# Kernel tuning notes

Hardware: AMD Instinct MI355X
Metric: run time of the kernel (lower is better)

The kernel has to match this reference:

```python
import jax, jax.numpy as jnp
import numpy as np

TOPK = 10
NUM_CLASSES = 80
ALPHA = 1.0
BETA = 6.0
EPS = 1e-9
IOU_EPS = 1e-7
IMG = 640.0


def setup_inputs() -> dict:
    key = jax.random.key(0)
    ks = jax.random.split(key, 8)
    B, N, M, C = 8, 16800, 96, NUM_CLASSES
    pd_scores = jax.random.normal(ks[0], (B, N, C), dtype=jnp.float32)
    # predicted boxes: valid xyxy around random centers
    p_c = jax.random.uniform(ks[1], (B, N, 2), dtype=jnp.float32) * IMG
    p_wh = jax.random.uniform(ks[2], (B, N, 2), dtype=jnp.float32) * (IMG / 8.0) + 1.0
    pd_bboxes = jnp.concatenate([p_c - p_wh / 2, p_c + p_wh / 2], axis=-1)
    anchor_points = jax.random.uniform(ks[3], (N, 2), dtype=jnp.float32) * IMG
    gt_labels = jax.random.randint(ks[4], (B, M, 1), 0, C, dtype=jnp.int32)
    g_c = jax.random.uniform(ks[5], (B, M, 2), dtype=jnp.float32) * IMG
    g_wh = jax.random.uniform(ks[6], (B, M, 2), dtype=jnp.float32) * (IMG / 4.0) + 4.0
    gt_bboxes = jnp.concatenate([g_c - g_wh / 2, g_c + g_wh / 2], axis=-1)
    # first 72 of 96 GT slots valid per image (padding mask)
    mask_gt = jnp.broadcast_to((jnp.arange(M) < 72).astype(jnp.float32)[None, :, None], (B, M, 1))
    return {"pd_scores": pd_scores, "pd_bboxes": pd_bboxes, "anchor_points": anchor_points,
            "gt_labels": gt_labels, "gt_bboxes": gt_bboxes, "mask_gt": mask_gt}


def _bbox_iou(b1, b2):
    # b1: (B,N,1,4), b2: (B,1,M,4) -> (B,N,M)
    ix1 = jnp.maximum(b1[..., 0], b2[..., 0])
    iy1 = jnp.maximum(b1[..., 1], b2[..., 1])
    ix2 = jnp.minimum(b1[..., 2], b2[..., 2])
    iy2 = jnp.minimum(b1[..., 3], b2[..., 3])
    inter = jnp.clip(ix2 - ix1, 0.0) * jnp.clip(iy2 - iy1, 0.0)
    a1 = (b1[..., 2] - b1[..., 0]) * (b1[..., 3] - b1[..., 1])
    a2 = (b2[..., 2] - b2[..., 0]) * (b2[..., 3] - b2[..., 1])
    return inter / (a1 + a2 - inter + IOU_EPS)


def _assign(pd_scores, pd_bboxes, anchor_points, gt_labels, gt_bboxes, mask_gt):
    B, N, C = pd_scores.shape
    M = gt_bboxes.shape[1]
    mg = mask_gt[:, :, 0]                      # (B,M)
    gl = gt_labels[:, :, 0].astype(jnp.int32)  # (B,M)

    # --- anchor centers inside GT boxes -> (B,N,M) ---
    lt = gt_bboxes[:, :, None, :2]             # (B,M,1,2)
    rb = gt_bboxes[:, :, None, 2:]
    ap = anchor_points[None, None, :, :]       # (1,1,N,2)
    deltas = jnp.concatenate([ap - lt, rb - ap], axis=-1)  # (B,M,N,4)
    mask_in_gts = jnp.swapaxes(deltas.min(-1) > EPS, 1, 2).astype(pd_scores.dtype)  # (B,N,M)

    # --- IoU + alignment metric ---
    overlaps = jnp.clip(_bbox_iou(pd_bboxes[:, :, None, :], gt_bboxes[:, None, :, :]), 0.0)  # (B,N,M)
    gl_exp = jnp.broadcast_to(gl[:, None, :], (B, N, M))
    bbox_scores = jnp.take_along_axis(pd_scores, gl_exp, axis=2)  # (B,N,M)
    align = (jax.nn.sigmoid(bbox_scores) ** ALPHA) * (overlaps ** BETA)
    align = align * mg[:, None, :]

    # --- top-k anchors per GT (over anchor axis) ---
    mT = jnp.swapaxes(align, 1, 2)                     # (B,M,N)
    topk_vals, topk_idxs = jax.lax.top_k(mT, min(TOPK, N))
    keep = topk_vals.max(-1, keepdims=True) > EPS       # (B,M,1)
    bi = jnp.arange(B)[:, None, None]
    mi = jnp.arange(M)[None, :, None]
    sel = jnp.zeros((B, M, N), dtype=bool).at[bi, mi, topk_idxs].set(True)
    mask_topk = jnp.swapaxes(sel & keep, 1, 2).astype(pd_scores.dtype)  # (B,N,M)

    mask_pos = mask_in_gts * mask_topk * mg[:, None, :]

    # --- resolve anchors assigned to multiple GTs by max IoU ---
    fg_count = mask_pos.sum(2)                          # (B,N)
    multi = (fg_count[:, :, None] > 1)
    is_max = jax.nn.one_hot(overlaps.argmax(2), M, dtype=overlaps.dtype)
    mask_pos = jnp.where(multi, is_max, mask_pos)
    fg_mask = mask_pos.sum(2) > 0                       # (B,N) bool
    target_gt_idx = mask_pos.argmax(2)                  # (B,N)

    # --- gather targets ---
    target_labels = jnp.take_along_axis(gl, target_gt_idx, axis=1)
    target_labels = jnp.clip(target_labels, 0, C - 1)
    target_bboxes = jnp.take_along_axis(gt_bboxes, target_gt_idx[:, :, None], axis=1)  # (B,N,4)

    # --- normalized alignment metric -> scores (faithful .long() truncation) ---
    max_per_gt = jnp.clip(align.max(1, keepdims=True), EPS)
    norm_align = (align / max_per_gt).max(2) * fg_mask.astype(align.dtype)  # (B,N)
    bi2 = jnp.arange(B)[:, None]
    ni = jnp.arange(N)[None, :]
    assigned = jnp.zeros((B, N, C), dtype=jnp.int32).at[bi2, ni, target_labels].set(
        norm_align.astype(jnp.int32))
    target_scores = jnp.where(fg_mask[:, :, None], assigned.astype(pd_scores.dtype),
                              jnp.zeros((), pd_scores.dtype))
    return target_bboxes, target_scores, fg_mask, target_gt_idx


def reference(pd_scores, pd_bboxes, anchor_points, gt_labels, gt_bboxes, mask_gt):
    return _assign(pd_scores, pd_bboxes, anchor_points, gt_labels, gt_bboxes, mask_gt)
```

## Files before the change

### kernel.cpp

```cpp
#include <hip/hip_runtime.h>
#include <math.h>

#define TOPK_K 10
#define EPS_F 1e-9f
#define IOU_EPS_F 1e-7f
#define CH 128
#define QH 4
#define CCH 256
#define MGMAX 32

struct Iou6 { float ov; float ov6; };

__device__ __forceinline__ Iou6 iou_pow6(float px1, float py1, float px2, float py2,
                                         float gx1, float gy1, float gx2, float gy2) {
#pragma clang fp contract(off)
  float ix1 = fmaxf(px1, gx1);
  float iy1 = fmaxf(py1, gy1);
  float ix2 = fminf(px2, gx2);
  float iy2 = fminf(py2, gy2);
  float dw = fmaxf(ix2 - ix1, 0.0f);
  float dh = fmaxf(iy2 - iy1, 0.0f);
  float inter = dw * dh;
  float a1 = (px2 - px1) * (py2 - py1);
  float a2 = (gx2 - gx1) * (gy2 - gy1);
  float den = a1 + a2 - inter + IOU_EPS_F;
  float iou = inter / den;
  float ov = fmaxf(iou, 0.0f);
  float ov2 = ov * ov;
  Iou6 r; r.ov = ov; r.ov6 = ov2 * ov2 * ov2;
  return r;
}

__device__ __forceinline__ float sigmoid_f(float x) {
#pragma clang fp contract(off)
  return 1.0f / (1.0f + expf(-x));
}

__device__ __forceinline__ unsigned long long mk_key(float v, int idx) {
  if (idx < 0) return 0ull;
  unsigned uv = __float_as_uint(v) | 0x80000000u;
  return ((unsigned long long)uv << 32) | (unsigned)(~idx);
}

#define KINSERT(kk)                                                      \
  if ((kk) > kl[9]) {                                                    \
    _Pragma("unroll")                                                    \
    for (int j = 9; j >= 1; --j) {                                       \
      if ((kk) > kl[j - 1])      kl[j] = kl[j - 1];                      \
      else if ((kk) > kl[j])     kl[j] = (kk);                           \
    }                                                                    \
    if ((kk) > kl[0]) kl[0] = (kk);                                      \
  }

#define WAVE_MERGE10()                                                         \
  {                                                                            \
    _Pragma("unroll")                                                          \
    for (int r = 0; r < TOPK_K; ++r) {                                         \
      unsigned long long kmine = kl[0], kw = kl[0];                            \
      _Pragma("unroll")                                                        \
      for (int off = 32; off > 0; off >>= 1) {                                 \
        unsigned long long o = __shfl_xor(kw, off);                            \
        if (o > kw) kw = o;                                                    \
      }                                                                        \
      if (lane == 0) skey[wid * TOPK_K + r] = kw;                              \
      if (kmine == kw && kw != 0ull) {                  \
        _Pragma("unroll")                                                      \
        for (int j = 0; j < TOPK_K - 1; ++j) kl[j] = kl[j + 1];                \
        kl[TOPK_K - 1] = 0ull;                                                 \
      }                                                                        \
    }                                                                          \
  }

#define FINAL_MERGE10()                                                        \
  {                                                                            \
    _Pragma("unroll")                                                          \
    for (int r = 0; r < TOPK_K; ++r) {                                         \
      unsigned long long kmine = kl[0], kw = kl[0];                            \
      _Pragma("unroll")                                                        \
      for (int off = 32; off > 0; off >>= 1) {                                 \
        unsigned long long o = __shfl_xor(kw, off);                            \
        if (o > kw) kw = o;                                                    \
      }                                                                        \
      if (r == 0) maxv = __uint_as_float((unsigned)(kw >> 32) & 0x7fffffffu);  \
      if (r == TOPK_K - 1) {                                                   \
        Tv = __uint_as_float((unsigned)(kw >> 32) & 0x7fffffffu);              \
        Ti = (int)~(unsigned)(kw & 0xffffffffu);                               \
      }                                                                        \
      if (kmine == kw && kw != 0ull) {                                         \
        _Pragma("unroll")                                                      \
        for (int j = 0; j < TOPK_K - 1; ++j) kl[j] = kl[j + 1];                \
        kl[TOPK_K - 1] = 0ull;                                                 \
      }                                                                        \
    }                                                                          \
  }

__launch_bounds__(CCH)
__global__ void k_collect(const float* __restrict__ pd_scores,
                          const float* __restrict__ pd_bboxes,
                          const int*   __restrict__ gt_labels,
                          const float* __restrict__ gt_bboxes,
                          const float* __restrict__ mask_gt,
                          int B, int N, int M, int C, int CAP, int MGS,
                          int*    __restrict__ cnt,
                          float2* __restrict__ lists)
{
  const int b = blockIdx.z;
  const int m0 = blockIdx.y * MGS;
  const int mcount = min(MGS, M - m0);
  const int tid = threadIdx.x;
  const int n = blockIdx.x * CCH + tid;
  const int lane = tid & 63;
  const int wid  = tid >> 6;
  const bool valid = (n < N);

  __shared__ float4             sgt[MGMAX];
  __shared__ int                sgl[MGMAX];
  __shared__ int                smg[MGMAX];
  __shared__ unsigned long long sbal[CCH / 64][MGMAX];
  __shared__ int                wbase[CCH / 64][MGMAX];

  if (tid < mcount) {
    sgt[tid] = *(const float4*)(gt_bboxes + (size_t)(b * M + m0 + tid) * 4);
    sgl[tid] = min(max(gt_labels[b * M + m0 + tid], 0), C - 1);
    smg[tid] = (mask_gt[b * M + m0 + tid] > 0.0f) ? 1 : 0;
  }
  __syncthreads();

  float4 p = make_float4(-1.f, -1.f, -2.f, -2.f);
  if (valid) p = *(const float4*)(pd_bboxes + ((size_t)b * N + n) * 4);

  for (int mi = 0; mi < mcount; ++mi) {
    const float4 g = sgt[mi];
    bool pred = false;
    if (smg[mi]) {
      float ix1 = fmaxf(p.x, g.x), iy1 = fmaxf(p.y, g.y);
      float ix2 = fminf(p.z, g.z), iy2 = fminf(p.w, g.w);
      pred = (ix2 > ix1) && (iy2 > iy1);
    }
    unsigned long long bal = __ballot(pred);
    if (lane == 0) sbal[wid][mi] = bal;
  }
  __syncthreads();

  if (tid < mcount) {
    int t0 = __popcll(sbal[0][tid]), t1 = __popcll(sbal[1][tid]);
    int t2 = __popcll(sbal[2][tid]), t3 = __popcll(sbal[3][tid]);
    int tot = t0 + t1 + t2 + t3;
    int gb = (tot > 0) ? atomicAdd(&cnt[b * M + m0 + tid], tot) : 0;
    wbase[0][tid] = gb;
    wbase[1][tid] = gb + t0;
    wbase[2][tid] = gb + t0 + t1;
    wbase[3][tid] = gb + t0 + t1 + t2;
  }
  __syncthreads();

  const float* __restrict__ srow = pd_scores + ((size_t)b * N + n) * C;
  const unsigned long long ltm = (1ull << lane) - 1ull;
  for (int mi = 0; mi < mcount; ++mi) {
    unsigned long long bal = sbal[wid][mi];
    if (bal == 0ull) continue;
    if ((bal >> lane) & 1ull) {
      int pos = wbase[wid][mi] + __popcll(bal & ltm);
      if (pos < CAP) {
        const float4 g = sgt[mi];
        Iou6 io = iou_pow6(p.x, p.y, p.z, p.w, g.x, g.y, g.z, g.w);
        float a = sigmoid_f(srow[sgl[mi]]) * io.ov6;
        lists[(size_t)(b * M + m0 + mi) * CAP + pos] = make_float2(a, __int_as_float(n));
      }
    }
  }
}

__launch_bounds__(256)
__global__ void k_select(const float* __restrict__ pd_scores,
                         const float* __restrict__ pd_bboxes,
                         const int*   __restrict__ gt_labels,
                         const float* __restrict__ gt_bboxes,
                         const float* __restrict__ mask_gt,
                         int B, int N, int M, int C, int CAP,
                         const int*    __restrict__ cnt,
                         const float2* __restrict__ lists,
                         float* __restrict__ maxv_out,
                         float* __restrict__ t10v_out,
                         int*   __restrict__ t10i_out)
{
  const int m = blockIdx.x, b = blockIdx.y;
  const int bm = b * M + m;
  const int tid = threadIdx.x;
  const int lane = tid & 63;
  const int wid  = tid >> 6;

  __shared__ unsigned long long skey[4 * TOPK_K];
  __shared__ int sfb;

  if (mask_gt[bm] == 0.0f) {
    if (tid == 0) { maxv_out[bm] = 0.0f; t10v_out[bm] = 0.0f; t10i_out[bm] = -1; }
    return;
  }

  unsigned long long kl[TOPK_K];
#pragma unroll
  for (int j = 0; j < TOPK_K; ++j) kl[j] = 0ull;

  float maxv = 0.0f, Tv = 0.0f; int Ti = -1;
  const int c = cnt[bm];
  bool fb = (c < TOPK_K) || (c > CAP);

  if (!fb) {
    const float2* __restrict__ lp = lists + (size_t)bm * CAP;
    for (int i = tid; i < c; i += 256) {
      float2 e = lp[i];
      unsigned long long k = mk_key(e.x, __float_as_int(e.y));
      KINSERT(k);
    }
    WAVE_MERGE10();
    __syncthreads();
    if (wid == 0) {
#pragma unroll
      for (int j = 0; j < TOPK_K; ++j) kl[j] = 0ull;
      kl[0] = (lane < 4 * TOPK_K) ? skey[lane] : 0ull;
      FINAL_MERGE10();
      if (lane == 0) sfb = (Tv == 0.0f) ? 1 : 0;
    }
    __syncthreads();
    fb = (sfb != 0);
  }

  if (fb) {
#pragma unroll
    for (int j = 0; j < TOPK_K; ++j) kl[j] = 0ull;
    const float4 g = *(const float4*)(gt_bboxes + (size_t)bm * 4);
    int gl = min(max(gt_labels[bm], 0), C - 1);
    const float* __restrict__ srow = pd_scores + (size_t)b * N * C;
    const float4* __restrict__ pb = (const float4*)(pd_bboxes + (size_t)b * N * 4);
    for (int n = tid; n < N; n += 256) {
      float4 p = pb[n];
      Iou6 io = iou_pow6(p.x, p.y, p.z, p.w, g.x, g.y, g.z, g.w);
      unsigned long long kub = mk_key(io.ov6, 0);
      if (kub > kl[TOPK_K - 1]) {
        float a = (io.ov6 == 0.0f) ? 0.0f
                                   : sigmoid_f(srow[(size_t)n * C + gl]) * io.ov6;
        unsigned long long k = mk_key(a, n);
        KINSERT(k);
      }
    }
    __syncthreads();
    WAVE_MERGE10();
    __syncthreads();
    if (wid == 0) {
#pragma unroll
      for (int j = 0; j < TOPK_K; ++j) kl[j] = 0ull;
      kl[0] = (lane < 4 * TOPK_K) ? skey[lane] : 0ull;
      FINAL_MERGE10();
    }
  }

  if (tid == 0) { maxv_out[bm] = maxv; t10v_out[bm] = Tv; t10i_out[bm] = Ti; }
}

__launch_bounds__(512)
__global__ void k_assign(const float* __restrict__ pd_scores,
                         const float* __restrict__ pd_bboxes,
                         const float* __restrict__ anchors,
                         const int*   __restrict__ gt_labels,
                         const float* __restrict__ gt_bboxes,
                         const float* __restrict__ mask_gt,
                         const float* __restrict__ maxv_in,
                         const float* __restrict__ t10v_in,
                         const int*   __restrict__ t10i_in,
                         int B, int N, int M, int C,
                         float* __restrict__ out)
{
  const int b = blockIdx.y;
  const int chunk0 = blockIdx.x * CH;
  const int tid = threadIdx.x;
  const int al = tid & (CH - 1);
  const int qr = tid >> 7;
  const int n = chunk0 + al;

  __shared__ float4 sgt[128];
  __shared__ int    sgl[128];
  __shared__ float  smg[128];
  __shared__ float  smpg[128];
  __shared__ float  spre[128];
  __shared__ float  smT[128];
  __shared__ int    smI[128];
  __shared__ int    skeep[128];
  __shared__ float  s_pov[QH - 1][CH];
  __shared__ int    s_parg[QH - 1][CH], s_pcnt[QH - 1][CH],
                    s_pfirst[QH - 1][CH], s_pone[QH - 1][CH];
  __shared__ int    slab[CH];
  __shared__ float  ssv[CH];

  if (tid < M) {
    sgt[tid] = *(const float4*)(gt_bboxes + (size_t)(b * M + tid) * 4);
    sgl[tid] = min(max(gt_labels[b * M + tid], 0), C - 1);
    smg[tid] = mask_gt[b * M + tid];
    float mv  = maxv_in[b * M + tid];
    float mpg = fmaxf(mv, EPS_F);
    smpg[tid] = mpg;
    spre[tid] = mpg * 0.999999f;
    smT[tid]  = t10v_in[b * M + tid];
    smI[tid]  = t10i_in[b * M + tid];
    skeep[tid] = (mv > EPS_F) ? 1 : 0;
  }
  __syncthreads();

  float* __restrict__ out_bbox   = out;
  float* __restrict__ out_scores = out + (size_t)B * N * 4;
  float* __restrict__ out_fg     = out_scores + (size_t)B * N * C;
  float* __restrict__ out_tgt    = out_fg + (size_t)B * N;

  const bool valid = (n < N);
  float pov = -1.0f; int parg = 0;
  int pcnt = 0, pfirst = -1, pone = 0;

  if (valid) {
    const float4 p = *(const float4*)(pd_bboxes + ((size_t)b * N + n) * 4);
    const float ax = anchors[(size_t)n * 2];
    const float ay = anchors[(size_t)n * 2 + 1];
    const float* __restrict__ srow = pd_scores + ((size_t)b * N + n) * C;

    const int mq  = (M + QH - 1) / QH;
    const int mlo = qr * mq;
    const int mhi = min(M, mlo + mq);

    for (int m = mlo; m < mhi; ++m) {
      const float4 gbb = sgt[m];
      Iou6 io = iou_pow6(p.x, p.y, p.z, p.w, gbb.x, gbb.y, gbb.z, gbb.w);
      if (io.ov > pov) { pov = io.ov; parg = m; }
      const float mgv = smg[m];
      if (mgv > 0.0f) {
        const float T = smT[m];
        const int keep = skeep[m];
        bool mem = false;
        const bool cand = keep && (io.ov6 > T);
        if (cand || (io.ov6 >= spre[m])) {
          const float a = sigmoid_f(srow[sgl[m]]) * io.ov6;
          if (cand) mem = (a > T) || (a == T && n <= smI[m]);
          if (a / smpg[m] >= 1.0f) pone = 1;
        } else if (keep && (T == 0.0f) && (io.ov6 == 0.0f)) {
          mem = (n <= smI[m]);
        }
        if (mem) {
          const float d = fminf(fminf(ax - gbb.x, ay - gbb.y),
                                fminf(gbb.z - ax, gbb.w - ay));
          if (d > EPS_F) { pcnt++; if (pfirst < 0) pfirst = m; }
        }
      }
    }
  }

  if (qr >= 1 && valid) {
    s_pov[qr - 1][al] = pov; s_parg[qr - 1][al] = parg; s_pcnt[qr - 1][al] = pcnt;
    s_pfirst[qr - 1][al] = pfirst; s_pone[qr - 1][al] = pone;
  }
  __syncthreads();

  if (qr == 0 && valid) {
#pragma unroll
    for (int q = 0; q < QH - 1; ++q) {
      float ovq = s_pov[q][al];
      if (ovq > pov) { pov = ovq; parg = s_parg[q][al]; }
      pcnt += s_pcnt[q][al];
      if (pfirst < 0) pfirst = s_pfirst[q][al];
      pone |= s_pone[q][al];
    }

    float fg; int tgt;
    if (pcnt > 1)       { fg = 1.0f; tgt = parg; }
    else if (pcnt == 1) { fg = 1.0f; tgt = pfirst; }
    else                { fg = 0.0f; tgt = 0; }

    slab[al] = sgl[tgt];
    ssv[al]  = (fg > 0.0f && pone) ? 1.0f : 0.0f;

    *(float4*)(out_bbox + ((size_t)b * N + n) * 4) = sgt[tgt];
    out_fg[(size_t)b * N + n]  = fg;
    out_tgt[(size_t)b * N + n] = (float)tgt;
  }
  __syncthreads();

  const int rows = min(CH, N - chunk0);
  const int c4n = C >> 2;
  float4* __restrict__ os4 = (float4*)(out_scores + ((size_t)b * N + chunk0) * C);
  const int tot = rows * c4n;
  if (c4n == 20) {
    for (int i = tid; i < tot; i += 512) {
      unsigned row = __umulhi((unsigned)i, 0xCCCCCCCDu) >> 4;
      int c0 = (i - (int)row * 20) * 4;
      int lr = slab[row]; float v = ssv[row];
      float4 o;
      o.x = (c0     == lr) ? v : 0.0f;
      o.y = (c0 + 1 == lr) ? v : 0.0f;
      o.z = (c0 + 2 == lr) ? v : 0.0f;
      o.w = (c0 + 3 == lr) ? v : 0.0f;
      os4[i] = o;
    }
  } else {
    for (int i = tid; i < tot; i += 512) {
      int row = i / c4n;
      int c0 = (i - row * c4n) * 4;
      int lr = slab[row]; float v = ssv[row];
      float4 o;
      o.x = (c0     == lr) ? v : 0.0f;
      o.y = (c0 + 1 == lr) ? v : 0.0f;
      o.z = (c0 + 2 == lr) ? v : 0.0f;
      o.w = (c0 + 3 == lr) ? v : 0.0f;
      os4[i] = o;
    }
  }
}

extern "C" void kernel_launch(void* const* d_in, const int* in_sizes, int n_in,
                              void* d_out, int out_size, void* d_ws, size_t ws_size,
                              hipStream_t stream) {
  const float* pd_scores = (const float*)d_in[0];
  const float* pd_bboxes = (const float*)d_in[1];
  const float* anchors   = (const float*)d_in[2];
  const int*   gt_labels = (const int*)d_in[3];
  const float* gt_bboxes = (const float*)d_in[4];
  const float* mask_gt   = (const float*)d_in[5];

  const int N = in_sizes[2] / 2;
  const int B = in_sizes[1] / (N * 4);
  const int M = in_sizes[3] / B;
  const int C = in_sizes[0] / (B * N);
  const int BM = B * M;

  char* ws = (char*)d_ws;
  float*  maxv  = (float*)ws;  ws += (size_t)BM * 4;
  float*  t10v  = (float*)ws;  ws += (size_t)BM * 4;
  int*    t10i  = (int*)ws;    ws += (size_t)BM * 4;
  int*    cnt   = (int*)ws;    ws += (size_t)BM * 4;
  float2* lists = (float2*)ws;

  const size_t header = (size_t)BM * 16;
  size_t avail = (ws_size > header) ? (ws_size - header) : 0;
  long long capll = (long long)(avail / ((size_t)BM * 8));
  int CAP = (int)((capll > 4096) ? 4096 : capll);
  if (CAP < 512) CAP = 0;

  hipMemsetAsync(cnt, 0, (size_t)BM * 4, stream);

  if (CAP > 0) {
    int MGRP = 4;
    int MGS  = (M + MGRP - 1) / MGRP;
    while (MGS > MGMAX) { MGRP *= 2; MGS = (M + MGRP - 1) / MGRP; }
    dim3 gc((N + CCH - 1) / CCH, MGRP, B);
    k_collect<<<gc, CCH, 0, stream>>>(pd_scores, pd_bboxes, gt_labels, gt_bboxes,
                                      mask_gt, B, N, M, C, CAP, MGS, cnt, lists);
  }

  dim3 gs(M, B);
  k_select<<<gs, 256, 0, stream>>>(pd_scores, pd_bboxes, gt_labels, gt_bboxes,
                                   mask_gt, B, N, M, C, CAP, cnt, lists,
                                   maxv, t10v, t10i);

  dim3 g2((N + CH - 1) / CH, B);
  k_assign<<<g2, 512, 0, stream>>>(pd_scores, pd_bboxes, anchors, gt_labels,
                                   gt_bboxes, mask_gt, maxv, t10v, t10i,
                                   B, N, M, C, (float*)d_out);
}
```

Before: 80.41 us.

## Replace atomic candidate lists with per-wave fixed slots in collect/select

The collect kernel no longer reserves space in each GT's candidate list with global atomicAdd, and the count-buffer memset is gone. Instead, each wavefront writes its candidates into a private 32-entry slot per GT and records its own count. This removes two block barriers, the atomics and one memset launch. The select kernel now walks the per-wave slots and counts, and falls back to a full scan when any slot overflows or there are too few candidates. The cost is a much larger workspace, a fallback if the workspace is too small, and uneven per-thread serial loops in select.

New measurement: 88.51 us. 10.1% more time.

```diff
diff --git a/kernel.cpp b/kernel.cpp
--- a/kernel.cpp
+++ b/kernel.cpp
@@ -8,6 +8,7 @@
 #define QH 4
 #define CCH 256
 #define MGMAX 32
+#define SLOT 32
 
 struct Iou6 { float ov; float ov6; };
 
@@ -100,8 +101,8 @@
                           const int*   __restrict__ gt_labels,
                           const float* __restrict__ gt_bboxes,
                           const float* __restrict__ mask_gt,
-                          int B, int N, int M, int C, int CAP, int MGS,
-                          int*    __restrict__ cnt,
+                          int B, int N, int M, int C, int MGS, int WPG,
+                          int*    __restrict__ wcount,
                           float2* __restrict__ lists)
 {
   const int b = blockIdx.z;
@@ -111,13 +112,11 @@
   const int n = blockIdx.x * CCH + tid;
   const int lane = tid & 63;
   const int wid  = tid >> 6;
-  const bool valid = (n < N);
-
-  __shared__ float4             sgt[MGMAX];
-  __shared__ int                sgl[MGMAX];
-  __shared__ int                smg[MGMAX];
-  __shared__ unsigned long long sbal[CCH / 64][MGMAX];
-  __shared__ int                wbase[CCH / 64][MGMAX];
+  const int slot = blockIdx.x * (CCH / 64) + wid;
+
+  __shared__ float4 sgt[MGMAX];
+  __shared__ int    sgl[MGMAX];
+  __shared__ int    smg[MGMAX];
 
   if (tid < mcount) {
     sgt[tid] = *(const float4*)(gt_bboxes + (size_t)(b * M + m0 + tid) * 4);
@@ -127,7 +126,10 @@
   __syncthreads();
 
   float4 p = make_float4(-1.f, -1.f, -2.f, -2.f);
-  if (valid) p = *(const float4*)(pd_bboxes + ((size_t)b * N + n) * 4);
+  if (n < N) p = *(const float4*)(pd_bboxes + ((size_t)b * N + n) * 4);
+
+  const float* __restrict__ srow = pd_scores + ((size_t)b * N + n) * C;
+  const unsigned long long ltm = (1ull << lane) - 1ull;
 
   for (int mi = 0; mi < mcount; ++mi) {
     const float4 g = sgt[mi];
@@ -138,34 +140,14 @@
       pred = (ix2 > ix1) && (iy2 > iy1);
     }
     unsigned long long bal = __ballot(pred);
-    if (lane == 0) sbal[wid][mi] = bal;
-  }
-  __syncthreads();
-
-  if (tid < mcount) {
-    int t0 = __popcll(sbal[0][tid]), t1 = __popcll(sbal[1][tid]);
-    int t2 = __popcll(sbal[2][tid]), t3 = __popcll(sbal[3][tid]);
-    int tot = t0 + t1 + t2 + t3;
-    int gb = (tot > 0) ? atomicAdd(&cnt[b * M + m0 + tid], tot) : 0;
-    wbase[0][tid] = gb;
-    wbase[1][tid] = gb + t0;
-    wbase[2][tid] = gb + t0 + t1;
-    wbase[3][tid] = gb + t0 + t1 + t2;
-  }
-  __syncthreads();
-
-  const float* __restrict__ srow = pd_scores + ((size_t)b * N + n) * C;
-  const unsigned long long ltm = (1ull << lane) - 1ull;
-  for (int mi = 0; mi < mcount; ++mi) {
-    unsigned long long bal = sbal[wid][mi];
-    if (bal == 0ull) continue;
-    if ((bal >> lane) & 1ull) {
-      int pos = wbase[wid][mi] + __popcll(bal & ltm);
-      if (pos < CAP) {
-        const float4 g = sgt[mi];
+    const size_t sbase = (size_t)(b * M + m0 + mi) * WPG + slot;
+    if (lane == 0 && slot < WPG) wcount[sbase] = __popcll(bal);
+    if (pred) {
+      int pos = __popcll(bal & ltm);
+      if (pos < SLOT) {
         Iou6 io = iou_pow6(p.x, p.y, p.z, p.w, g.x, g.y, g.z, g.w);
         float a = sigmoid_f(srow[sgl[mi]]) * io.ov6;
-        lists[(size_t)(b * M + m0 + mi) * CAP + pos] = make_float2(a, __int_as_float(n));
+        lists[sbase * SLOT + pos] = make_float2(a, __int_as_float(n));
       }
     }
   }
@@ -177,8 +159,8 @@
                          const int*   __restrict__ gt_labels,
                          const float* __restrict__ gt_bboxes,
                          const float* __restrict__ mask_gt,
-                         int B, int N, int M, int C, int CAP,
-                         const int*    __restrict__ cnt,
+                         int B, int N, int M, int C, int WPG,
+                         const int*    __restrict__ wcount,
                          const float2* __restrict__ lists,
                          float* __restrict__ maxv_out,
                          float* __restrict__ t10v_out,
@@ -191,7 +173,7 @@
   const int wid  = tid >> 6;
 
   __shared__ unsigned long long skey[4 * TOPK_K];
-  __shared__ int sfb;
+  __shared__ int sTot, sOvf, sfb;
 
   if (mask_gt[bm] == 0.0f) {
     if (tid == 0) { maxv_out[bm] = 0.0f; t10v_out[bm] = 0.0f; t10i_out[bm] = -1; }
@@ -203,27 +185,42 @@
   for (int j = 0; j < TOPK_K; ++j) kl[j] = 0ull;
 
   float maxv = 0.0f, Tv = 0.0f; int Ti = -1;
-  const int c = cnt[bm];
-  bool fb = (c < TOPK_K) || (c > CAP);
+  bool fb = (WPG <= 0);
 
   if (!fb) {
-    const float2* __restrict__ lp = lists + (size_t)bm * CAP;
-    for (int i = tid; i < c; i += 256) {
-      float2 e = lp[i];
-      unsigned long long k = mk_key(e.x, __float_as_int(e.y));
-      KINSERT(k);
-    }
-    WAVE_MERGE10();
+    if (tid == 0) { sTot = 0; sOvf = 0; }
     __syncthreads();
-    if (wid == 0) {
+    int mytot = 0, myovf = 0;
+    for (int s = tid; s < WPG; s += 256) {
+      int c = wcount[(size_t)bm * WPG + s];
+      mytot += c;
+      if (c > SLOT) myovf = 1;
+      const float2* __restrict__ lp = lists + ((size_t)bm * WPG + s) * SLOT;
+      int cc = min(c, SLOT);
+      for (int i = 0; i < cc; ++i) {
+        float2 e = lp[i];
+        unsigned long long k = mk_key(e.x, __float_as_int(e.y));
+        KINSERT(k);
+      }
+    }
+    if (mytot) atomicAdd(&sTot, mytot);
+    if (myovf) atomicOr(&sOvf, 1);
+    __syncthreads();
+    if (sTot >= TOPK_K && !sOvf) {
+      WAVE_MERGE10();
+      __syncthreads();
+      if (wid == 0) {
 #pragma unroll
-      for (int j = 0; j < TOPK_K; ++j) kl[j] = 0ull;
-      kl[0] = (lane < 4 * TOPK_K) ? skey[lane] : 0ull;
-      FINAL_MERGE10();
-      if (lane == 0) sfb = (Tv == 0.0f) ? 1 : 0;
-    }
-    __syncthreads();
-    fb = (sfb != 0);
+        for (int j = 0; j < TOPK_K; ++j) kl[j] = 0ull;
+        kl[0] = (lane < 4 * TOPK_K) ? skey[lane] : 0ull;
+        FINAL_MERGE10();
+        if (lane == 0) sfb = (Tv == 0.0f) ? 1 : 0;
+      }
+      __syncthreads();
+      fb = (sfb != 0);
+    } else {
+      fb = true;
+    }
   }
 
   if (fb) {
@@ -428,33 +425,32 @@
   const int C = in_sizes[0] / (B * N);
   const int BM = B * M;
 
+  int WPG = (N + 63) / 64;
+
   char* ws = (char*)d_ws;
-  float*  maxv  = (float*)ws;  ws += (size_t)BM * 4;
-  float*  t10v  = (float*)ws;  ws += (size_t)BM * 4;
-  int*    t10i  = (int*)ws;    ws += (size_t)BM * 4;
-  int*    cnt   = (int*)ws;    ws += (size_t)BM * 4;
-  float2* lists = (float2*)ws;
-
-  const size_t header = (size_t)BM * 16;
-  size_t avail = (ws_size > header) ? (ws_size - header) : 0;
-  long long capll = (long long)(avail / ((size_t)BM * 8));
-  int CAP = (int)((capll > 4096) ? 4096 : capll);
-  if (CAP < 512) CAP = 0;
-
-  hipMemsetAsync(cnt, 0, (size_t)BM * 4, stream);
-
-  if (CAP > 0) {
+  float*  maxv   = (float*)ws;  ws += (size_t)BM * 4;
+  float*  t10v   = (float*)ws;  ws += (size_t)BM * 4;
+  int*    t10i   = (int*)ws;    ws += (size_t)BM * 4;
+  int*    wcnt   = (int*)ws;    ws += (size_t)BM * WPG * 4;
+  ws = (char*)(((uintptr_t)ws + 7) & ~(uintptr_t)7);
+  float2* lists  = (float2*)ws;
+
+  const size_t need = (size_t)BM * 12 + (size_t)BM * WPG * 4 + 8
+                    + (size_t)BM * WPG * SLOT * 8;
+  if (need > ws_size) WPG = 0;
+
+  if (WPG > 0) {
     int MGRP = 4;
     int MGS  = (M + MGRP - 1) / MGRP;
     while (MGS > MGMAX) { MGRP *= 2; MGS = (M + MGRP - 1) / MGRP; }
     dim3 gc((N + CCH - 1) / CCH, MGRP, B);
     k_collect<<<gc, CCH, 0, stream>>>(pd_scores, pd_bboxes, gt_labels, gt_bboxes,
-                                      mask_gt, B, N, M, C, CAP, MGS, cnt, lists);
+                                      mask_gt, B, N, M, C, MGS, WPG, wcnt, lists);
   }
 
   dim3 gs(M, B);
   k_select<<<gs, 256, 0, stream>>>(pd_scores, pd_bboxes, gt_labels, gt_bboxes,
-                                   mask_gt, B, N, M, C, CAP, cnt, lists,
+                                   mask_gt, B, N, M, C, WPG, wcnt, lists,
                                    maxv, t10v, t10i);
 
   dim3 g2((N + CH - 1) / CH, B);
```
